# Kernel optimization log

Hardware: AMD Instinct MI355X
Metric: run time of the kernel (lower is better)

## Reference

```python
import jax, jax.numpy as jnp
import numpy as np

B, N, E = 8, 10000, 160000
D_IN, D_H = 128, 128
EPS = 1e-5


def setup_inputs() -> dict:
    key = jax.random.key(0)
    ks = jax.random.split(key, 10)
    x = jax.random.normal(ks[0], (B, N, D_IN), dtype=jnp.float32)
    h_prev = jax.random.normal(ks[1], (B, N, D_H), dtype=jnp.float32)
    edge_index = jax.random.randint(ks[2], (2, E), 0, N, dtype=jnp.int32)
    d_cat = D_IN + D_H
    s = 1.0 / np.sqrt(d_cat)
    def w(k):
        return jax.random.uniform(k, (d_cat, D_H), jnp.float32, -s, s)
    def b(k):
        return jax.random.uniform(k, (D_H,), jnp.float32, -s, s)
    return {
        "x": x, "edge_index": edge_index, "h_prev": h_prev,
        "Wz": w(ks[3]), "bz": b(ks[4]),
        "Wr": w(ks[5]), "br": b(ks[6]),
        "Wc": w(ks[7]), "bc": b(ks[8]),
        "gamma": jnp.ones((D_H,), jnp.float32),
        "beta": jnp.zeros((D_H,), jnp.float32),
    }


def _gcn(x, W, bias, src, dst, norm, n_nodes):
    # PyG GCNConv: linear transform, gather from src, weight by sym-norm, scatter-add to dst
    msg = (x @ W)[src] * norm[:, None]          # [E_total, D_H]
    return jax.ops.segment_sum(msg, dst, num_segments=n_nodes) + bias


def reference(x, edge_index, h_prev, Wz, bz, Wr, br, Wc, bc, gamma, beta):
    Bx, Nx, _ = x.shape
    BN = Bx * Nx
    x_flat = x.reshape(BN, -1)
    h_flat = h_prev.reshape(BN, -1)

    # batch the edge index with per-graph node offsets (all edges are in-range)
    offsets = (jnp.arange(Bx, dtype=edge_index.dtype) * Nx)[:, None]
    src = (edge_index[0][None, :] + offsets).reshape(-1)
    dst = (edge_index[1][None, :] + offsets).reshape(-1)

    # GCN self-loops + symmetric normalization (shared by all three convs)
    loops = jnp.arange(BN, dtype=src.dtype)
    src = jnp.concatenate([src, loops])
    dst = jnp.concatenate([dst, loops])
    deg = jax.ops.segment_sum(jnp.ones_like(dst, dtype=x.dtype), dst, num_segments=BN)
    dis = jnp.where(deg > 0, 1.0 / jnp.sqrt(jnp.maximum(deg, 1.0)), 0.0)
    norm = dis[src] * dis[dst]

    xh = jnp.concatenate([x_flat, h_flat], axis=1)
    z = jax.nn.sigmoid(_gcn(xh, Wz, bz, src, dst, norm, BN))
    r = jax.nn.sigmoid(_gcn(xh, Wr, br, src, dst, norm, BN))
    xrh = jnp.concatenate([x_flat, r * h_flat], axis=1)
    h_cand = jnp.tanh(_gcn(xrh, Wc, bc, src, dst, norm, BN))

    h_new = (1.0 - z) * h_flat + z * h_cand

    # LayerNorm over last dim
    mu = h_new.mean(axis=-1, keepdims=True)
    var = ((h_new - mu) ** 2).mean(axis=-1, keepdims=True)
    h_new = (h_new - mu) / jnp.sqrt(var + EPS) * gamma + beta
    return h_new.reshape(Bx, Nx, -1)
```

## Files before the change

kernel.cpp:

```cpp
#include <hip/hip_runtime.h>

#define NN 10000
#define BB 8
#define EE 160000
#define DH 128
#define LN_EPS 1e-5f

typedef unsigned short ushort_t;
typedef unsigned int uint_t;

typedef __bf16 bf16x8 __attribute__((ext_vector_type(8)));
typedef float floatx4 __attribute__((ext_vector_type(4)));
typedef float floatx2 __attribute__((ext_vector_type(2)));

__device__ __forceinline__ float b2f(uint_t u) { return __uint_as_float(u << 16); }
__device__ __forceinline__ ushort_t f2b(float f) {
    uint_t u = __float_as_uint(f);
    return (ushort_t)((u + 0x7fffu + ((u >> 16) & 1u)) >> 16);
}
__device__ __forceinline__ uint_t pack2(float lo, float hi) {
    return (uint_t)f2b(lo) | ((uint_t)f2b(hi) << 16);
}
__device__ __forceinline__ float sigm(float x) { return 1.0f / (1.0f + __expf(-x)); }
__device__ __forceinline__ float tanh_fast(float x) {
    float ex = __expf(2.0f * x);
    return 1.0f - 2.0f / (ex + 1.0f);
}

__device__ __forceinline__ floatx2 unpk(uint_t u) {
    floatx2 r;
    r.x = __uint_as_float(u << 16);
    r.y = __uint_as_float(u & 0xffff0000u);
    return r;
}
__device__ __forceinline__ void pk_fma(floatx2& a, floatx2 w, floatx2 v) {
    asm("v_pk_fma_f32 %0, %1, %2, %0" : "+v"(a) : "v"(w), "v"(v));
}
__device__ __forceinline__ void acc8p(floatx2* a, floatx2 w2, uint4 v) {
    pk_fma(a[0], w2, unpk(v.x));
    pk_fma(a[1], w2, unpk(v.y));
    pk_fma(a[2], w2, unpk(v.z));
    pk_fma(a[3], w2, unpk(v.w));
}


__global__ void count_deg(const int* __restrict__ ei, int* __restrict__ cnt) {
    int e = blockIdx.x * 256 + threadIdx.x;
    if (e < EE) atomicAdd(&cnt[ei[EE + e]], 1);
}

__global__ __launch_bounds__(256) void scan1(const int* __restrict__ cnt,
                                             int* __restrict__ offs,
                                             int* __restrict__ bsum) {
    __shared__ int s[256];
    const int t = threadIdx.x, idx = blockIdx.x * 256 + t;
    int x = (idx < NN) ? cnt[idx] : 0;
    s[t] = x;
    __syncthreads();
    for (int o = 1; o < 256; o <<= 1) {
        int v = s[t];
        int u = (t >= o) ? s[t - o] : 0;
        __syncthreads();
        s[t] = v + u;
        __syncthreads();
    }
    if (idx < NN) offs[idx] = s[t] - x;
    if (t == 255) bsum[blockIdx.x] = s[255];
}

__global__ __launch_bounds__(256) void scan3(const int* __restrict__ cnt,
                                             const int* __restrict__ bsum,
                                             int* __restrict__ offs,
                                             int* __restrict__ cursor,
                                             float* __restrict__ dis) {
    __shared__ int sb[40];
    __shared__ int pfx;
    const int t = threadIdx.x;
    if (t < 40) sb[t] = bsum[t];
    __syncthreads();
    if (t == 0) {
        int a = 0;
        for (int i = 0; i < blockIdx.x; ++i) a += sb[i];
        pfx = a;
    }
    __syncthreads();
    const int idx = blockIdx.x * 256 + t;
    if (idx < NN) {
        int off = offs[idx] + pfx;
        offs[idx] = off;
        cursor[idx] = off;
        dis[idx] = rsqrtf((float)(cnt[idx] + 1));
    }
    if (idx == 0) offs[NN] = EE;
}

__global__ void fill_csr(const int* __restrict__ ei, int* __restrict__ cursor,
                         const float* __restrict__ dis, int* __restrict__ csr_src,
                         ushort_t* __restrict__ csr_w) {
    int e = blockIdx.x * 256 + threadIdx.x;
    if (e < EE) {
        int s = ei[e];
        int d = ei[EE + e];
        int pos = atomicAdd(&cursor[d], 1);
        csr_src[pos] = s;
        csr_w[pos] = f2b(dis[s]);
    }
}


__global__ __launch_bounds__(256) void packwt_k(const float* __restrict__ x,
                                                const float* __restrict__ h,
                                                ushort_t* __restrict__ xb,
                                                ushort_t* __restrict__ hb,
                                                const float* __restrict__ Wz,
                                                const float* __restrict__ Wr,
                                                const float* __restrict__ Wc,
                                                ushort_t* __restrict__ Wt_zr,
                                                ushort_t* __restrict__ Wt_c) {
    if (blockIdx.x < 10000) {
        const size_t o = ((size_t)blockIdx.x * 256 + threadIdx.x) * 4;
        float4 vx = *(const float4*)(x + o);
        uint2 px;
        px.x = pack2(vx.x, vx.y);
        px.y = pack2(vx.z, vx.w);
        *(uint2*)(xb + o) = px;
        float4 vh = *(const float4*)(h + o);
        uint2 ph;
        ph.x = pack2(vh.x, vh.y);
        ph.y = pack2(vh.z, vh.w);
        *(uint2*)(hb + o) = ph;
    } else {
        const int col = blockIdx.x - 10000, k = threadIdx.x;
        if (col < 256) {
            float v = (col < 128) ? Wz[(size_t)k * 128 + col]
                                  : Wr[(size_t)k * 128 + col - 128];
            Wt_zr[(size_t)col * 256 + k] = f2b(v);
        } else {
            int c2 = col - 256;
            Wt_c[(size_t)c2 * 256 + k] = f2b(Wc[(size_t)k * 128 + c2]);
        }
    }
}


template <int NB>
__global__ __launch_bounds__(256) void gather4(
    const ushort_t* __restrict__ src0, const ushort_t* __restrict__ src1,
    const int* __restrict__ offs, const int* __restrict__ csr_src,
    const ushort_t* __restrict__ csr_w, const float* __restrict__ dis,
    ushort_t* __restrict__ dst0, ushort_t* __restrict__ dst1) {
    const int tid = threadIdx.x, lane = tid & 63;
    const int b = blockIdx.x & 7;
    const int n = (blockIdx.x >> 3) * 4 + (tid >> 6);
    const int g = lane >> 4, il = lane & 15;
    const ushort_t* base0 = src0 + (size_t)b * NN * 128;
    const ushort_t* base1 = (NB == 2) ? (src1 + (size_t)b * NN * 128) : base0;

    floatx2 a0[4], a1[4];
#pragma unroll
    for (int j = 0; j < 4; ++j) {
        a0[j] = (floatx2){0.f, 0.f};
        a1[j] = (floatx2){0.f, 0.f};
    }

    const float dn = dis[n];
    if (g == 0) {
        const floatx2 d2 = {dn, dn};
        const uint_t off = (uint_t)n * 128u + (uint_t)il * 8u;
        uint4 v = *(const uint4*)(base0 + off);
        acc8p(a0, d2, v);
        if (NB == 2) {
            uint4 vv = *(const uint4*)(base1 + off);
            acc8p(a1, d2, vv);
        }
    }

    const int e0 = offs[n], e1 = offs[n + 1];
    for (int ch = e0; ch < e1; ch += 64) {
        const int rem = e1 - ch;
        int idx = 0, wb = 0;
        if (lane < rem) {
            idx = csr_src[ch + lane];
            wb = (int)((uint_t)csr_w[ch + lane] << 16);
        }
        const int m = rem < 64 ? rem : 64;
        const int groups = (m + 3) >> 2;
        int pidx = g * 4;
#pragma unroll 4
        for (int i = 0; i < groups; ++i) {
            const int s = __builtin_amdgcn_ds_bpermute(pidx, idx);
            const float w =
                __uint_as_float((uint_t)__builtin_amdgcn_ds_bpermute(pidx, wb));
            pidx += 16;
            const floatx2 w2 = {w, w};
            const uint_t off = (uint_t)s * 128u + (uint_t)il * 8u;
            uint4 v = *(const uint4*)(base0 + off);
            acc8p(a0, w2, v);
            if (NB == 2) {
                uint4 vv = *(const uint4*)(base1 + off);
                acc8p(a1, w2, vv);
            }
        }
    }

    float o0[8], o1[8];
#pragma unroll
    for (int j = 0; j < 4; ++j) {
        o0[2 * j] = a0[j].x;
        o0[2 * j + 1] = a0[j].y;
        o1[2 * j] = a1[j].x;
        o1[2 * j + 1] = a1[j].y;
    }
#pragma unroll
    for (int j = 0; j < 8; ++j) {
        o0[j] *= dn;
        o0[j] += __shfl_xor(o0[j], 16);
        o0[j] += __shfl_xor(o0[j], 32);
    }
    if (NB == 2) {
#pragma unroll
        for (int j = 0; j < 8; ++j) {
            o1[j] *= dn;
            o1[j] += __shfl_xor(o1[j], 16);
            o1[j] += __shfl_xor(o1[j], 32);
        }
    }

    if (lane < 16) {
        const size_t o = ((size_t)b * NN + n) * 128 + (size_t)il * 8;
        uint4 st;
        st.x = pack2(o0[0], o0[1]);
        st.y = pack2(o0[2], o0[3]);
        st.z = pack2(o0[4], o0[5]);
        st.w = pack2(o0[6], o0[7]);
        *(uint4*)(dst0 + o) = st;
        if (NB == 2) {
            uint4 st1;
            st1.x = pack2(o1[0], o1[1]);
            st1.y = pack2(o1[2], o1[3]);
            st1.z = pack2(o1[4], o1[5]);
            st1.w = pack2(o1[6], o1[7]);
            *(uint4*)(dst1 + o) = st1;
        }
    }
}


template <int PHASE>
__global__ __launch_bounds__(256) void gemm_k(
    const ushort_t* __restrict__ A1, const ushort_t* __restrict__ A2,
    const ushort_t* __restrict__ Wt, const float* __restrict__ bz,
    const float* __restrict__ br, const float* __restrict__ bc,
    const float* __restrict__ h_prev, const ushort_t* __restrict__ z_in,
    const float* __restrict__ gamma, const float* __restrict__ beta,
    ushort_t* __restrict__ z_out, ushort_t* __restrict__ rh_out,
    float* __restrict__ f_out) {
    __shared__ __align__(16) ushort_t As[128 * 72];
    __shared__ __align__(16) ushort_t Bs[128 * 72];
    const int tid = threadIdx.x;
    const int rb0 = blockIdx.x * 128;
    const int mode = (PHASE == 1) ? 2 : blockIdx.y;
    const int cb0 = (mode == 1) ? 128 : 0;

    const int wv = tid >> 6, lane = tid & 63;
    const int l15 = lane & 15, q = lane >> 4;
    const int sr = tid >> 1;
    const int kh = (tid & 1) * 32;

    floatx4 acc[2][8];
#pragma unroll
    for (int i = 0; i < 2; ++i)
#pragma unroll
        for (int j = 0; j < 8; ++j) acc[i][j] = (floatx4){0.f, 0.f, 0.f, 0.f};

    for (int k0 = 0; k0 < 256; k0 += 64) {
        {
            const int kg = k0 + kh;
            const ushort_t* s = (kg < 128) ? (A1 + (size_t)(rb0 + sr) * 128 + kg)
                                           : (A2 + (size_t)(rb0 + sr) * 128 + (kg - 128));
            ushort_t* dst = &As[sr * 72 + kh];
#pragma unroll
            for (int i = 0; i < 4; ++i) *(uint4*)(dst + i * 8) = *(const uint4*)(s + i * 8);
        }
        {
            const ushort_t* s = Wt + (size_t)(cb0 + sr) * 256 + k0 + kh;
            ushort_t* dst = &Bs[sr * 72 + kh];
#pragma unroll
            for (int i = 0; i < 4; ++i) *(uint4*)(dst + i * 8) = *(const uint4*)(s + i * 8);
        }
        __syncthreads();
#pragma unroll
        for (int ks = 0; ks < 2; ++ks) {
            const int ko = ks * 32 + q * 8;
            bf16x8 a0 = *(const bf16x8*)&As[(wv * 32 + l15) * 72 + ko];
            bf16x8 a1 = *(const bf16x8*)&As[(wv * 32 + 16 + l15) * 72 + ko];
#pragma unroll
            for (int j = 0; j < 8; ++j) {
                bf16x8 b = *(const bf16x8*)&Bs[(j * 16 + l15) * 72 + ko];
                acc[0][j] = __builtin_amdgcn_mfma_f32_16x16x32_bf16(a0, b, acc[0][j], 0, 0, 0);
                acc[1][j] = __builtin_amdgcn_mfma_f32_16x16x32_bf16(a1, b, acc[1][j], 0, 0, 0);
            }
        }
        __syncthreads();
    }

    if (mode == 0) {
        float bv[8];
#pragma unroll
        for (int j = 0; j < 8; ++j) bv[j] = bz[j * 16 + l15];
#pragma unroll
        for (int i = 0; i < 2; ++i)
#pragma unroll
            for (int j = 0; j < 8; ++j)
#pragma unroll
                for (int v = 0; v < 4; ++v) {
                    int row = rb0 + wv * 32 + i * 16 + q * 4 + v;
                    z_out[(size_t)row * 128 + j * 16 + l15] = f2b(sigm(acc[i][j][v] + bv[j]));
                }
    } else if (mode == 1) {
        float bv[8];
#pragma unroll
        for (int j = 0; j < 8; ++j) bv[j] = br[j * 16 + l15];
#pragma unroll
        for (int i = 0; i < 2; ++i)
#pragma unroll
            for (int j = 0; j < 8; ++j)
#pragma unroll
                for (int v = 0; v < 4; ++v) {
                    int row = rb0 + wv * 32 + i * 16 + q * 4 + v;
                    float r = sigm(acc[i][j][v] + bv[j]);
                    float hh = h_prev[(size_t)row * 128 + j * 16 + l15];
                    rh_out[(size_t)row * 128 + j * 16 + l15] = f2b(r * hh);
                }
    } else {
        float bv[8], gv[8], bev[8];
#pragma unroll
        for (int j = 0; j < 8; ++j) {
            bv[j] = bc[j * 16 + l15];
            gv[j] = gamma[j * 16 + l15];
            bev[j] = beta[j * 16 + l15];
        }
#pragma unroll
        for (int i = 0; i < 2; ++i)
#pragma unroll
            for (int v = 0; v < 4; ++v) {
                const int row = rb0 + wv * 32 + i * 16 + q * 4 + v;
                float hn[8];
                float s = 0.f;
#pragma unroll
                for (int j = 0; j < 8; ++j) {
                    float hc = tanh_fast(acc[i][j][v] + bv[j]);
                    float zz = b2f((uint_t)z_in[(size_t)row * 128 + j * 16 + l15]);
                    float hh = h_prev[(size_t)row * 128 + j * 16 + l15];
                    hn[j] = (1.0f - zz) * hh + zz * hc;
                    s += hn[j];
                }
#pragma unroll
                for (int o = 8; o > 0; o >>= 1) s += __shfl_xor(s, o);
                float mu = s * (1.0f / 128.0f);
                float vv = 0.f;
#pragma unroll
                for (int j = 0; j < 8; ++j) {
                    float d = hn[j] - mu;
                    vv += d * d;
                }
#pragma unroll
                for (int o = 8; o > 0; o >>= 1) vv += __shfl_xor(vv, o);
                float inv = rsqrtf(vv * (1.0f / 128.0f) + LN_EPS);
#pragma unroll
                for (int j = 0; j < 8; ++j)
                    f_out[(size_t)row * 128 + j * 16 + l15] =
                        (hn[j] - mu) * inv * gv[j] + bev[j];
            }
    }
}


extern "C" void kernel_launch(void* const* d_in, const int* in_sizes, int n_in,
                              void* d_out, int out_size, void* d_ws, size_t ws_size,
                              hipStream_t stream) {
    const float* x = (const float*)d_in[0];
    const int* ei = (const int*)d_in[1];
    const float* h = (const float*)d_in[2];
    const float* Wz = (const float*)d_in[3];
    const float* bz = (const float*)d_in[4];
    const float* Wr = (const float*)d_in[5];
    const float* br = (const float*)d_in[6];
    const float* Wc = (const float*)d_in[7];
    const float* bcv = (const float*)d_in[8];
    const float* gamma = (const float*)d_in[9];
    const float* beta = (const float*)d_in[10];
    float* out = (float*)d_out;

    char* w = (char*)d_ws;
    int* offs = (int*)(w + 0);
    float* dis = (float*)(w + 40960);
    int* csr_src = (int*)(w + 81920);
    ushort_t* csr_w = (ushort_t*)(w + 721920);
    ushort_t* Wt_zr = (ushort_t*)(w + 1041920);
    ushort_t* Wt_c = (ushort_t*)(w + 1172992);
    ushort_t* xb = (ushort_t*)(w + 1239040);
    ushort_t* hb = (ushort_t*)(w + 21719040);
    ushort_t* agg_x = (ushort_t*)(w + 42199040);
    ushort_t* agg_h = (ushort_t*)(w + 62679040);
    int* cnt = (int*)(w + 1239040);
    int* cursor = (int*)(w + 1280000);
    int* bsum = (int*)(w + 1320000);
    ushort_t* z_buf = xb;
    ushort_t* rh_bf = hb;
    ushort_t* agg_rh = agg_h;

    hipMemsetAsync(cnt, 0, NN * sizeof(int), stream);
    count_deg<<<EE / 256, 256, 0, stream>>>(ei, cnt);
    scan1<<<40, 256, 0, stream>>>(cnt, offs, bsum);
    scan3<<<40, 256, 0, stream>>>(cnt, bsum, offs, cursor, dis);
    fill_csr<<<EE / 256, 256, 0, stream>>>(ei, cursor, dis, csr_src, csr_w);
    packwt_k<<<10384, 256, 0, stream>>>(x, h, xb, hb, Wz, Wr, Wc, Wt_zr, Wt_c);

    gather4<2><<<(BB * NN) / 4, 256, 0, stream>>>(xb, hb, offs, csr_src, csr_w, dis,
                                                  agg_x, agg_h);
    gemm_k<0><<<dim3(80000 / 128, 2), 256, 0, stream>>>(
        agg_x, agg_h, Wt_zr, bz, br, bcv, h, (const ushort_t*)0, gamma, beta,
        z_buf, rh_bf, (float*)0);
    gather4<1><<<(BB * NN) / 4, 256, 0, stream>>>(rh_bf, (const ushort_t*)0, offs,
                                                  csr_src, csr_w, dis, agg_rh,
                                                  (ushort_t*)0);
    gemm_k<1><<<dim3(80000 / 128, 1), 256, 0, stream>>>(
        agg_x, agg_rh, Wt_c, bz, br, bcv, h, z_buf, gamma, beta,
        (ushort_t*)0, (ushort_t*)0, out);
}
```

Measured before the change: 330.0 us.

## Use 512-thread GEMM blocks with register-prefetched double-staged tile loads

The GEMM kernel now runs 8 waves per block, each owning 16 rows instead of 32, which halves per-wave accumulators and raises the number of waves resident per CU. Global loads for the next K tile are issued into registers before the MFMA loop on the current tile, so load latency overlaps compute. The trade-off is the same LDS footprint shared by more threads and an extra barrier per K step, while the weight tile is still reloaded per block.

```diff
diff --git a/kernel.cpp b/kernel.cpp
--- a/kernel.cpp
+++ b/kernel.cpp
@@ -247,7 +247,7 @@
 
 
 template <int PHASE>
-__global__ __launch_bounds__(256) void gemm_k(
+__global__ __launch_bounds__(512) void gemm_k(
     const ushort_t* __restrict__ A1, const ushort_t* __restrict__ A2,
     const ushort_t* __restrict__ Wt, const float* __restrict__ bz,
     const float* __restrict__ br, const float* __restrict__ bc,
@@ -264,74 +264,74 @@
 
     const int wv = tid >> 6, lane = tid & 63;
     const int l15 = lane & 15, q = lane >> 4;
-    const int sr = tid >> 1;
-    const int kh = (tid & 1) * 32;
-
-    floatx4 acc[2][8];
-#pragma unroll
-    for (int i = 0; i < 2; ++i)
-#pragma unroll
-        for (int j = 0; j < 8; ++j) acc[i][j] = (floatx4){0.f, 0.f, 0.f, 0.f};
-
-    for (int k0 = 0; k0 < 256; k0 += 64) {
-        {
-            const int kg = k0 + kh;
-            const ushort_t* s = (kg < 128) ? (A1 + (size_t)(rb0 + sr) * 128 + kg)
-                                           : (A2 + (size_t)(rb0 + sr) * 128 + (kg - 128));
-            ushort_t* dst = &As[sr * 72 + kh];
-#pragma unroll
-            for (int i = 0; i < 4; ++i) *(uint4*)(dst + i * 8) = *(const uint4*)(s + i * 8);
-        }
-        {
-            const ushort_t* s = Wt + (size_t)(cb0 + sr) * 256 + k0 + kh;
-            ushort_t* dst = &Bs[sr * 72 + kh];
-#pragma unroll
-            for (int i = 0; i < 4; ++i) *(uint4*)(dst + i * 8) = *(const uint4*)(s + i * 8);
-        }
+    const int sr = tid >> 2;
+    const int kh = (tid & 3) * 16;
+
+    floatx4 acc[8];
+#pragma unroll
+    for (int j = 0; j < 8; ++j) acc[j] = (floatx4){0.f, 0.f, 0.f, 0.f};
+
+    uint4 pa0, pa1, pb0, pb1;
+#define LOAD_AB(k0)                                                                   \
+    {                                                                                 \
+        const int kg = (k0) + kh;                                                     \
+        const ushort_t* sA = (kg < 128)                                               \
+                                 ? (A1 + (size_t)(rb0 + sr) * 128 + kg)               \
+                                 : (A2 + (size_t)(rb0 + sr) * 128 + (kg - 128));      \
+        pa0 = *(const uint4*)(sA);                                                    \
+        pa1 = *(const uint4*)(sA + 8);                                                \
+        const ushort_t* sB = Wt + (size_t)(cb0 + sr) * 256 + (k0) + kh;               \
+        pb0 = *(const uint4*)(sB);                                                    \
+        pb1 = *(const uint4*)(sB + 8);                                                \
+    }
+
+    LOAD_AB(0);
+#pragma unroll
+    for (int t = 0; t < 4; ++t) {
+        if (t) __syncthreads();
+        *(uint4*)(&As[sr * 72 + kh]) = pa0;
+        *(uint4*)(&As[sr * 72 + kh + 8]) = pa1;
+        *(uint4*)(&Bs[sr * 72 + kh]) = pb0;
+        *(uint4*)(&Bs[sr * 72 + kh + 8]) = pb1;
         __syncthreads();
+        if (t < 3) LOAD_AB((t + 1) * 64);
 #pragma unroll
         for (int ks = 0; ks < 2; ++ks) {
             const int ko = ks * 32 + q * 8;
-            bf16x8 a0 = *(const bf16x8*)&As[(wv * 32 + l15) * 72 + ko];
-            bf16x8 a1 = *(const bf16x8*)&As[(wv * 32 + 16 + l15) * 72 + ko];
+            bf16x8 a0 = *(const bf16x8*)&As[(wv * 16 + l15) * 72 + ko];
 #pragma unroll
             for (int j = 0; j < 8; ++j) {
                 bf16x8 b = *(const bf16x8*)&Bs[(j * 16 + l15) * 72 + ko];
-                acc[0][j] = __builtin_amdgcn_mfma_f32_16x16x32_bf16(a0, b, acc[0][j], 0, 0, 0);
-                acc[1][j] = __builtin_amdgcn_mfma_f32_16x16x32_bf16(a1, b, acc[1][j], 0, 0, 0);
-            }
-        }
-        __syncthreads();
-    }
+                acc[j] = __builtin_amdgcn_mfma_f32_16x16x32_bf16(a0, b, acc[j], 0, 0, 0);
+            }
+        }
+    }
+#undef LOAD_AB
 
     if (mode == 0) {
         float bv[8];
 #pragma unroll
         for (int j = 0; j < 8; ++j) bv[j] = bz[j * 16 + l15];
 #pragma unroll
-        for (int i = 0; i < 2; ++i)
-#pragma unroll
-            for (int j = 0; j < 8; ++j)
-#pragma unroll
-                for (int v = 0; v < 4; ++v) {
-                    int row = rb0 + wv * 32 + i * 16 + q * 4 + v;
-                    z_out[(size_t)row * 128 + j * 16 + l15] = f2b(sigm(acc[i][j][v] + bv[j]));
-                }
+        for (int j = 0; j < 8; ++j)
+#pragma unroll
+            for (int v = 0; v < 4; ++v) {
+                int row = rb0 + wv * 16 + q * 4 + v;
+                z_out[(size_t)row * 128 + j * 16 + l15] = f2b(sigm(acc[j][v] + bv[j]));
+            }
     } else if (mode == 1) {
         float bv[8];
 #pragma unroll
         for (int j = 0; j < 8; ++j) bv[j] = br[j * 16 + l15];
 #pragma unroll
-        for (int i = 0; i < 2; ++i)
-#pragma unroll
-            for (int j = 0; j < 8; ++j)
-#pragma unroll
-                for (int v = 0; v < 4; ++v) {
-                    int row = rb0 + wv * 32 + i * 16 + q * 4 + v;
-                    float r = sigm(acc[i][j][v] + bv[j]);
-                    float hh = h_prev[(size_t)row * 128 + j * 16 + l15];
-                    rh_out[(size_t)row * 128 + j * 16 + l15] = f2b(r * hh);
-                }
+        for (int j = 0; j < 8; ++j)
+#pragma unroll
+            for (int v = 0; v < 4; ++v) {
+                int row = rb0 + wv * 16 + q * 4 + v;
+                float r = sigm(acc[j][v] + bv[j]);
+                float hh = h_prev[(size_t)row * 128 + j * 16 + l15];
+                rh_out[(size_t)row * 128 + j * 16 + l15] = f2b(r * hh);
+            }
     } else {
         float bv[8], gv[8], bev[8];
 #pragma unroll
@@ -341,37 +341,35 @@
             bev[j] = beta[j * 16 + l15];
         }
 #pragma unroll
-        for (int i = 0; i < 2; ++i)
-#pragma unroll
-            for (int v = 0; v < 4; ++v) {
-                const int row = rb0 + wv * 32 + i * 16 + q * 4 + v;
-                float hn[8];
-                float s = 0.f;
-#pragma unroll
-                for (int j = 0; j < 8; ++j) {
-                    float hc = tanh_fast(acc[i][j][v] + bv[j]);
-                    float zz = b2f((uint_t)z_in[(size_t)row * 128 + j * 16 + l15]);
-                    float hh = h_prev[(size_t)row * 128 + j * 16 + l15];
-                    hn[j] = (1.0f - zz) * hh + zz * hc;
-                    s += hn[j];
-                }
-#pragma unroll
-                for (int o = 8; o > 0; o >>= 1) s += __shfl_xor(s, o);
-                float mu = s * (1.0f / 128.0f);
-                float vv = 0.f;
-#pragma unroll
-                for (int j = 0; j < 8; ++j) {
-                    float d = hn[j] - mu;
-                    vv += d * d;
-                }
-#pragma unroll
-                for (int o = 8; o > 0; o >>= 1) vv += __shfl_xor(vv, o);
-                float inv = rsqrtf(vv * (1.0f / 128.0f) + LN_EPS);
-#pragma unroll
-                for (int j = 0; j < 8; ++j)
-                    f_out[(size_t)row * 128 + j * 16 + l15] =
-                        (hn[j] - mu) * inv * gv[j] + bev[j];
-            }
+        for (int v = 0; v < 4; ++v) {
+            const int row = rb0 + wv * 16 + q * 4 + v;
+            float hn[8];
+            float s = 0.f;
+#pragma unroll
+            for (int j = 0; j < 8; ++j) {
+                float hc = tanh_fast(acc[j][v] + bv[j]);
+                float zz = b2f((uint_t)z_in[(size_t)row * 128 + j * 16 + l15]);
+                float hh = h_prev[(size_t)row * 128 + j * 16 + l15];
+                hn[j] = (1.0f - zz) * hh + zz * hc;
+                s += hn[j];
+            }
+#pragma unroll
+            for (int o = 8; o > 0; o >>= 1) s += __shfl_xor(s, o);
+            float mu = s * (1.0f / 128.0f);
+            float vv = 0.f;
+#pragma unroll
+            for (int j = 0; j < 8; ++j) {
+                float d = hn[j] - mu;
+                vv += d * d;
+            }
+#pragma unroll
+            for (int o = 8; o > 0; o >>= 1) vv += __shfl_xor(vv, o);
+            float inv = rsqrtf(vv * (1.0f / 128.0f) + LN_EPS);
+#pragma unroll
+            for (int j = 0; j < 8; ++j)
+                f_out[(size_t)row * 128 + j * 16 + l15] =
+                    (hn[j] - mu) * inv * gv[j] + bev[j];
+        }
     }
 }
 
@@ -419,13 +417,13 @@
 
     gather4<2><<<(BB * NN) / 4, 256, 0, stream>>>(xb, hb, offs, csr_src, csr_w, dis,
                                                   agg_x, agg_h);
-    gemm_k<0><<<dim3(80000 / 128, 2), 256, 0, stream>>>(
+    gemm_k<0><<<dim3(80000 / 128, 2), 512, 0, stream>>>(
         agg_x, agg_h, Wt_zr, bz, br, bcv, h, (const ushort_t*)0, gamma, beta,
         z_buf, rh_bf, (float*)0);
     gather4<1><<<(BB * NN) / 4, 256, 0, stream>>>(rh_bf, (const ushort_t*)0, offs,
                                                   csr_src, csr_w, dis, agg_rh,
                                                   (ushort_t*)0);
-    gemm_k<1><<<dim3(80000 / 128, 1), 256, 0, stream>>>(
+    gemm_k<1><<<dim3(80000 / 128, 1), 512, 0, stream>>>(
         agg_x, agg_rh, Wt_c, bz, br, bcv, h, z_buf, gamma, beta,
         (ushort_t*)0, (ushort_t*)0, out);
 }
```

Result: faster. 316.7 us (-4.0%).
